# Kernel optimization log

Hardware: AMD Instinct MI355X
Metric: run time of the kernel (lower is better)

The kernel has to match this reference:

```python
import jax, jax.numpy as jnp
import numpy as np

N_HEAD = 16
N_KV_HEAD = 4
HEAD_DIM = 64
VE_CH = 12  # min(12, n_embd)


def apply_rotary_emb(x, cos, sin):
    d = x.shape[3] // 2
    x1, x2 = x[..., :d], x[..., d:]
    return jnp.concatenate([x1 * cos + x2 * sin, x1 * -sin + x2 * cos], axis=3)


def rms_norm(x):
    return x * jax.lax.rsqrt(jnp.mean(jnp.square(x), axis=-1, keepdims=True) + 1e-6)


def setup_inputs() -> dict:
    key = jax.random.key(0)
    ks = jax.random.split(key, 9)
    B, T, C = 2, 2048, 1024
    s = 0.02
    return {
        "x": jax.random.normal(ks[0], (B, T, C), jnp.float32),
        "ve": jax.random.normal(ks[1], (B, T, N_KV_HEAD * HEAD_DIM), jnp.float32),
        "cos": jax.random.normal(ks[2], (1, T, 1, HEAD_DIM // 2), jnp.float32),
        "sin": jax.random.normal(ks[3], (1, T, 1, HEAD_DIM // 2), jnp.float32),
        "Wq": jax.random.normal(ks[4], (C, C), jnp.float32) * s,
        "Wk": jax.random.normal(ks[5], (N_KV_HEAD * HEAD_DIM, C), jnp.float32) * s,
        "Wv": jax.random.normal(ks[6], (N_KV_HEAD * HEAD_DIM, C), jnp.float32) * s,
        "Wo": jax.random.normal(ks[7], (C, C), jnp.float32) * s,
        "Wg": jax.random.normal(ks[8], (N_KV_HEAD, VE_CH), jnp.float32) * s,
    }


def reference(x, ve, cos, sin, Wq, Wk, Wv, Wo, Wg):
    B, T, C = x.shape
    q = (x @ Wq.T).reshape(B, T, N_HEAD, HEAD_DIM)
    k = (x @ Wk.T).reshape(B, T, N_KV_HEAD, HEAD_DIM)
    v = (x @ Wv.T).reshape(B, T, N_KV_HEAD, HEAD_DIM)

    # value-embedding gate
    ve_r = ve.reshape(B, T, N_KV_HEAD, HEAD_DIM)
    gate = 3.0 * jax.nn.sigmoid(x[..., :VE_CH] @ Wg.T)  # [B,T,n_kv_head]
    v = v + gate[..., None] * ve_r

    q = apply_rotary_emb(q, cos, sin)
    k = apply_rotary_emb(k, cos, sin)
    q = rms_norm(q) * 1.2
    k = rms_norm(k) * 1.2

    # GQA: expand kv heads
    r = N_HEAD // N_KV_HEAD
    k = jnp.repeat(k, r, axis=2)
    v = jnp.repeat(v, r, axis=2)

    # [B,H,T,D]
    q = q.transpose(0, 2, 1, 3)
    k = k.transpose(0, 2, 1, 3)
    v = v.transpose(0, 2, 1, 3)

    scale = 1.0 / np.sqrt(HEAD_DIM).astype(np.float32)
    scores = jnp.einsum("bhqd,bhkd->bhqk", q, k) * scale
    causal = jnp.tril(jnp.ones((T, T), dtype=bool))
    scores = jnp.where(causal, scores, jnp.float32(-jnp.inf))
    att = jax.nn.softmax(scores, axis=-1)
    y = jnp.einsum("bhqk,bhkd->bhqd", att, v)
    y = y.transpose(0, 2, 1, 3).reshape(B, T, C)
    return y @ Wo.T
```

## Files before the change

kernel.cpp:

```cpp
#include <hip/hip_runtime.h>
#include <stdint.h>

#define B_SZ 2
#define T_SZ 2048
#define C_SZ 1024
#define NH   16
#define NKV  4
#define HD   64
#define KVD  256
#define QKV_N 1536

typedef __attribute__((ext_vector_type(8))) short bf16x8;
typedef __attribute__((ext_vector_type(4))) float f32x4;

#define GL(p) ((const __attribute__((address_space(1))) void*)(p))
#define LD(p) ((__attribute__((address_space(3))) void*)(p))

__device__ inline unsigned short f2bf(float f) {
  union { float f; unsigned u; } v; v.f = f;
  unsigned u = v.u;
  unsigned r = (u + 0x7fffu + ((u >> 16) & 1u)) >> 16;
  return (unsigned short)r;
}
__device__ inline unsigned short bftrunc(float f) {
  union { float f; unsigned u; } v; v.f = f;
  return (unsigned short)(v.u >> 16);
}

struct CvtArgs {
  const float *s0, *s1, *s2, *s3, *s4;
  unsigned short *d0, *d1, *d2, *d3, *d4;
  const float *x, *Wg;
  float *gate;
};
__global__ __launch_bounds__(256) void cvt_all(CvtArgs a) {
  int blk = blockIdx.x, tid = threadIdx.x;
  if (blk >= 6656) {
    int idx = (blk - 6656) * 256 + tid;
    int bt = idx >> 2, kh = idx & 3;
    float s = 0.f;
#pragma unroll
    for (int j = 0; j < 12; j++) s += a.x[(size_t)bt * C_SZ + j] * a.Wg[kh * 12 + j];
    a.gate[idx] = 3.f / (1.f + __expf(-s));
    return;
  }
  const float* s; unsigned short* d; int i;
  if      (blk < 4096) { s = a.s0; d = a.d0; i = blk * 256 + tid; }
  else if (blk < 5120) { s = a.s1; d = a.d1; i = (blk - 4096) * 256 + tid; }
  else if (blk < 5376) { s = a.s2; d = a.d2; i = (blk - 5120) * 256 + tid; }
  else if (blk < 5632) { s = a.s3; d = a.d3; i = (blk - 5376) * 256 + tid; }
  else                 { s = a.s4; d = a.d4; i = (blk - 5632) * 256 + tid; }
  float4 f = ((const float4*)s)[i];
  ushort4 o;
  o.x = f2bf(f.x); o.y = f2bf(f.y); o.z = f2bf(f.z); o.w = f2bf(f.w);
  ((ushort4*)d)[i] = o;
}

#define GEMM_PROLOG(A, Bm, K)                                                        \
  __shared__ unsigned short As[4][64 * 32];                                          \
  __shared__ unsigned short Bs[4][128 * 32];                                         \
  int tid  = threadIdx.x;                                                            \
  int lane = tid & 63;                                                               \
  int wave = tid >> 6;                                                               \
  int quad = lane >> 4;                                                              \
  int l16  = lane & 15;                                                              \
  int m0 = blockIdx.y * 64;                                                          \
  int n0 = blockIdx.x * 128;                                                         \
  int wm = (wave & 1) * 32;                                                          \
  int wn = (wave >> 1) * 64;                                                         \
  f32x4 acc[2][4];                                                                   \
  _Pragma("unroll") for (int i = 0; i < 2; i++)                                      \
    _Pragma("unroll") for (int j = 0; j < 4; j++)                                    \
      acc[i][j] = (f32x4){0.f, 0.f, 0.f, 0.f};                                       \
  int lrow = lane >> 2;                                                              \
  int lcol = (lane & 3) * 8;                                                         \
  int srowA = wave * 16;                                                             \
  int srowB = wave * 32;                                                             \
  const unsigned short* aP  = &A[(size_t)(m0 + srowA + lrow) * K + lcol];            \
  const unsigned short* b0P = &Bm[(size_t)(n0 + srowB + lrow) * K + lcol];           \
  const unsigned short* b1P = b0P + 16 * (size_t)K;                                  \
  for (int k0 = 0; k0 < K; k0 += 128) {                                              \
    __syncthreads();                                                                 \
    _Pragma("unroll") for (int p = 0; p < 4; p++) {                                  \
      __builtin_amdgcn_global_load_lds(GL(aP  + k0 + p * 32), LD(&As[p][srowA * 32]),        16, 0, 0); \
      __builtin_amdgcn_global_load_lds(GL(b0P + k0 + p * 32), LD(&Bs[p][srowB * 32]),        16, 0, 0); \
      __builtin_amdgcn_global_load_lds(GL(b1P + k0 + p * 32), LD(&Bs[p][(srowB + 16) * 32]), 16, 0, 0); \
    }                                                                                \
    __syncthreads();                                                                 \
    _Pragma("unroll") for (int p = 0; p < 4; p++) {                                  \
      bf16x8 af[2], bfr[4];                                                          \
      _Pragma("unroll") for (int i = 0; i < 2; i++)                                  \
        af[i] = *(const bf16x8*)&As[p][(wm + i * 16 + l16) * 32 + quad * 8];         \
      _Pragma("unroll") for (int j = 0; j < 4; j++)                                  \
        bfr[j] = *(const bf16x8*)&Bs[p][(wn + j * 16 + l16) * 32 + quad * 8];        \
      _Pragma("unroll") for (int i = 0; i < 2; i++)                                  \
        _Pragma("unroll") for (int j = 0; j < 4; j++)                                \
          acc[i][j] = __builtin_amdgcn_mfma_f32_16x16x32_bf16(af[i], bfr[j], acc[i][j], 0, 0, 0); \
    }                                                                                \
  }

__global__ __launch_bounds__(256) void gemm_bt(const unsigned short* __restrict__ A,
                                               const unsigned short* __restrict__ Bm,
                                               float* __restrict__ C,
                                               int N, int K) {
  GEMM_PROLOG(A, Bm, K)
#pragma unroll
  for (int i = 0; i < 2; i++) {
#pragma unroll
    for (int j = 0; j < 4; j++) {
      int col = n0 + wn + j * 16 + l16;
#pragma unroll
      for (int r = 0; r < 4; r++) {
        int row = m0 + wm + i * 16 + quad * 4 + r;
        C[(size_t)row * N + col] = acc[i][j][r];
      }
    }
  }
}

__global__ __launch_bounds__(256) void gemm_qkv(const unsigned short* __restrict__ A,
                                                const unsigned short* __restrict__ Bm,
                                                const float* __restrict__ ve,
                                                const float* __restrict__ cosb,
                                                const float* __restrict__ sinb,
                                                const float* __restrict__ gateArr,
                                                unsigned short* __restrict__ qa,
                                                unsigned short* __restrict__ ka,
                                                unsigned short* __restrict__ vtmp) {
  const int K = C_SZ;
  GEMM_PROLOG(A, Bm, K)

  int colbase = n0 + wn;
  if (colbase < 1280) {
    int isQ = colbase < 1024;
    int h   = isQ ? (colbase >> 6) : ((colbase - 1024) >> 6);
    float scale = isQ ? (0.15f * 1.44269504088896f) : 1.2f;
    unsigned short* dst = isQ ? qa : ka;
    int nheads = isQ ? NH : NKV;
#pragma unroll
    for (int i = 0; i < 2; i++) {
#pragma unroll
      for (int r = 0; r < 4; r++) {
        int row = m0 + wm + i * 16 + quad * 4 + r;
        int t = row & (T_SZ - 1), b = row >> 11;
        float a10 = acc[i][0][r], a11 = acc[i][1][r];
        float a20 = acc[i][2][r], a21 = acc[i][3][r];
        float cv0 = cosb[t * 32 + l16],      sv0 = sinb[t * 32 + l16];
        float cv1 = cosb[t * 32 + 16 + l16], sv1 = sinb[t * 32 + 16 + l16];
        float o10 =  a10 * cv0 + a20 * sv0;
        float o11 =  a11 * cv1 + a21 * sv1;
        float o20 = -a10 * sv0 + a20 * cv0;
        float o21 = -a11 * sv1 + a21 * cv1;
        float ssq = o10 * o10 + o11 * o11 + o20 * o20 + o21 * o21;
        ssq += __shfl_xor(ssq, 1);
        ssq += __shfl_xor(ssq, 2);
        ssq += __shfl_xor(ssq, 4);
        ssq += __shfl_xor(ssq, 8);
        float rn = rsqrtf(ssq * (1.f / 64.f) + 1e-6f) * scale;
        size_t base = ((size_t)(b * nheads + h) * T_SZ + t) * HD;
        dst[base + l16]      = f2bf(o10 * rn);
        dst[base + 16 + l16] = f2bf(o11 * rn);
        dst[base + 32 + l16] = f2bf(o20 * rn);
        dst[base + 48 + l16] = f2bf(o21 * rn);
      }
    }
  } else {
    int kh = (colbase - 1280) >> 6;
#pragma unroll
    for (int i = 0; i < 2; i++) {
#pragma unroll
      for (int r = 0; r < 4; r++) {
        int row = m0 + wm + i * 16 + quad * 4 + r;
        float g = gateArr[row * 4 + kh];
#pragma unroll
        for (int j = 0; j < 4; j++) {
          int d = j * 16 + l16;
          float val = acc[i][j][r] + g * ve[(size_t)row * KVD + kh * HD + d];
          vtmp[(size_t)row * KVD + kh * HD + d] = f2bf(val);
        }
      }
    }
  }
}

__global__ __launch_bounds__(256) void v_transpose(const unsigned short* __restrict__ vtmp,
                                                   unsigned short* __restrict__ vt) {
  __shared__ unsigned short tile[64 * 68];
  int blk = blockIdx.x;
  int tb = blk & 31, kh = (blk >> 5) & 3, b = blk >> 7;
  int tid = threadIdx.x;
  int r = tid >> 2, c = (tid & 3) * 16;
  const unsigned short* src = &vtmp[((size_t)(b * T_SZ + tb * 64 + r)) * KVD + kh * HD + c];
  uint4 x0 = *(const uint4*)(src);
  uint4 x1 = *(const uint4*)(src + 8);
  *(uint2*)&tile[r * 68 + c]      = *(uint2*)&x0;
  *(uint2*)&tile[r * 68 + c + 4]  = *((uint2*)&x0 + 1);
  *(uint2*)&tile[r * 68 + c + 8]  = *(uint2*)&x1;
  *(uint2*)&tile[r * 68 + c + 12] = *((uint2*)&x1 + 1);
  __syncthreads();
  int d = tid >> 2, tc = (tid & 3) * 16;
  ushort4 o0, o1, o2, o3;
  o0.x = tile[(tc + 0) * 68 + d];  o0.y = tile[(tc + 1) * 68 + d];
  o0.z = tile[(tc + 2) * 68 + d];  o0.w = tile[(tc + 3) * 68 + d];
  o1.x = tile[(tc + 4) * 68 + d];  o1.y = tile[(tc + 5) * 68 + d];
  o1.z = tile[(tc + 6) * 68 + d];  o1.w = tile[(tc + 7) * 68 + d];
  o2.x = tile[(tc + 8) * 68 + d];  o2.y = tile[(tc + 9) * 68 + d];
  o2.z = tile[(tc + 10) * 68 + d]; o2.w = tile[(tc + 11) * 68 + d];
  o3.x = tile[(tc + 12) * 68 + d]; o3.y = tile[(tc + 13) * 68 + d];
  o3.z = tile[(tc + 14) * 68 + d]; o3.w = tile[(tc + 15) * 68 + d];
  unsigned short* dst = &vt[((size_t)(b * NKV + kh) * HD + d) * T_SZ + tb * 64 + tc];
  *(ushort4*)(dst)      = o0;
  *(ushort4*)(dst + 4)  = o1;
  *(ushort4*)(dst + 8)  = o2;
  *(ushort4*)(dst + 12) = o3;
}

#define KST 72
#define PST 72
__global__ __launch_bounds__(256) void attn(const unsigned short* __restrict__ qa,
                                            const unsigned short* __restrict__ ka,
                                            const unsigned short* __restrict__ vt,
                                            unsigned short* __restrict__ y) {
  int bid = blockIdx.x;
  int half = bid >> 8, r = bid & 255;
  int qt = half ? (r & 15) : 15 - (r & 15);
  int bh = (half << 4) | (r >> 4);
  int b = bh >> 4, h = bh & 15;
  int kh = h >> 2;
  int tid = threadIdx.x;
  int wave = tid >> 6, lane = tid & 63;
  int quad = lane >> 4, l16 = lane & 15;

  __shared__ unsigned short Ks[2][64 * KST];
  __shared__ unsigned short Vs[2][64 * KST];
  __shared__ unsigned short Ps[128 * PST];
  unsigned short* Pw = &Ps[(wave * 32) * PST];

  bf16x8 bq[2][2];
#pragma unroll
  for (int qi = 0; qi < 2; qi++) {
    int tq = qt * 128 + wave * 32 + qi * 16 + l16;
    const unsigned short* qp = &qa[((size_t)(b * NH + h) * T_SZ + tq) * HD];
    bq[qi][0] = *(const bf16x8*)&qp[quad * 8];
    bq[qi][1] = *(const bf16x8*)&qp[32 + quad * 8];
  }

  const unsigned short one_bf = 0x3F80;
  bf16x8 vones = {(short)one_bf, (short)one_bf, (short)one_bf, (short)one_bf,
                  (short)one_bf, (short)one_bf, (short)one_bf, (short)one_bf};

  f32x4 oacc[2][4];
  f32x4 lacc[2];
#pragma unroll
  for (int qi = 0; qi < 2; qi++) {
    lacc[qi] = (f32x4){0.f, 0.f, 0.f, 0.f};
#pragma unroll
    for (int d = 0; d < 4; d++) oacc[qi][d] = (f32x4){0.f, 0.f, 0.f, 0.f};
  }

  int lr = tid >> 2;
  int lc = (tid & 3) * 16;

  const unsigned short* kbase = &ka[(size_t)(b * NKV + kh) * T_SZ * HD];
  const unsigned short* vbase = &vt[(size_t)(b * NKV + kh) * HD * T_SZ];

  int nj = 2 * qt + 2;

  {
    const unsigned short* kp = &kbase[(size_t)lr * HD + lc];
    const unsigned short* vp = &vbase[(size_t)lr * T_SZ + lc];
    uint4 k0 = *(const uint4*)(kp);
    uint4 k1 = *(const uint4*)(kp + 8);
    uint4 v0 = *(const uint4*)(vp);
    uint4 v1 = *(const uint4*)(vp + 8);
    *(uint4*)&Ks[0][lr * KST + lc]     = k0;
    *(uint4*)&Ks[0][lr * KST + lc + 8] = k1;
    *(uint4*)&Vs[0][lr * KST + lc]     = v0;
    *(uint4*)&Vs[0][lr * KST + lc + 8] = v1;
  }

  int qrow0 = qt * 128 + wave * 32;

  for (int j = 0; j < nj; j++) {
    int cur = j & 1, nxt = cur ^ 1;
    __syncthreads();

    uint4 k0, k1, v0, v1;
    bool pf = (j + 1 < nj);
    if (pf) {
      const unsigned short* kp = &kbase[(size_t)((j + 1) * 64 + lr) * HD + lc];
      const unsigned short* vp = &vbase[(size_t)lr * T_SZ + (j + 1) * 64 + lc];
      k0 = *(const uint4*)(kp);
      k1 = *(const uint4*)(kp + 8);
      v0 = *(const uint4*)(vp);
      v1 = *(const uint4*)(vp + 8);
    }

    f32x4 st[4][2];
#pragma unroll
    for (int tb = 0; tb < 4; tb++) {
      bf16x8 ak0 = *(const bf16x8*)&Ks[cur][(tb * 16 + l16) * KST + quad * 8];
      bf16x8 ak1 = *(const bf16x8*)&Ks[cur][(tb * 16 + l16) * KST + 32 + quad * 8];
#pragma unroll
      for (int qi = 0; qi < 2; qi++) {
        f32x4 s = (f32x4){0.f, 0.f, 0.f, 0.f};
        s = __builtin_amdgcn_mfma_f32_16x16x32_bf16(ak0, bq[qi][0], s, 0, 0, 0);
        s = __builtin_amdgcn_mfma_f32_16x16x32_bf16(ak1, bq[qi][1], s, 0, 0, 0);
        st[tb][qi] = s;
      }
    }

#pragma unroll
    for (int qi = 0; qi < 2; qi++) {
      int qlow = qrow0 + qi * 16;
      if (j * 64 + 63 > qlow) {
        int qg = qlow + l16;
#pragma unroll
        for (int tb = 0; tb < 4; tb++) {
          int tg = j * 64 + tb * 16 + quad * 4;
#pragma unroll
          for (int i = 0; i < 4; i++) {
            if (tg + i > qg) st[tb][qi][i] = -__builtin_inff();
          }
        }
      }
#pragma unroll
      for (int tb = 0; tb < 4; tb++) {
        ushort4 w;
        w.x = bftrunc(__builtin_amdgcn_exp2f(st[tb][qi][0]));
        w.y = bftrunc(__builtin_amdgcn_exp2f(st[tb][qi][1]));
        w.z = bftrunc(__builtin_amdgcn_exp2f(st[tb][qi][2]));
        w.w = bftrunc(__builtin_amdgcn_exp2f(st[tb][qi][3]));
        *(ushort4*)&Pw[(qi * 16 + l16) * PST + tb * 16 + quad * 4] = w;
      }
    }

    bf16x8 ap[2][2];
#pragma unroll
    for (int qi = 0; qi < 2; qi++) {
      ap[qi][0] = *(const bf16x8*)&Pw[(qi * 16 + l16) * PST + quad * 8];
      ap[qi][1] = *(const bf16x8*)&Pw[(qi * 16 + l16) * PST + 32 + quad * 8];
      lacc[qi] = __builtin_amdgcn_mfma_f32_16x16x32_bf16(ap[qi][0], vones, lacc[qi], 0, 0, 0);
      lacc[qi] = __builtin_amdgcn_mfma_f32_16x16x32_bf16(ap[qi][1], vones, lacc[qi], 0, 0, 0);
    }
#pragma unroll
    for (int d = 0; d < 4; d++) {
      bf16x8 bv0 = *(const bf16x8*)&Vs[cur][(d * 16 + l16) * KST + quad * 8];
      bf16x8 bv1 = *(const bf16x8*)&Vs[cur][(d * 16 + l16) * KST + 32 + quad * 8];
#pragma unroll
      for (int qi = 0; qi < 2; qi++) {
        oacc[qi][d] = __builtin_amdgcn_mfma_f32_16x16x32_bf16(ap[qi][0], bv0, oacc[qi][d], 0, 0, 0);
        oacc[qi][d] = __builtin_amdgcn_mfma_f32_16x16x32_bf16(ap[qi][1], bv1, oacc[qi][d], 0, 0, 0);
      }
    }

    if (pf) {
      *(uint4*)&Ks[nxt][lr * KST + lc]     = k0;
      *(uint4*)&Ks[nxt][lr * KST + lc + 8] = k1;
      *(uint4*)&Vs[nxt][lr * KST + lc]     = v0;
      *(uint4*)&Vs[nxt][lr * KST + lc + 8] = v1;
    }
  }

#pragma unroll
  for (int qi = 0; qi < 2; qi++) {
#pragma unroll
    for (int i = 0; i < 4; i++) {
      int tq = qrow0 + qi * 16 + quad * 4 + i;
      float inv = 1.f / lacc[qi][i];
#pragma unroll
      for (int d = 0; d < 4; d++) {
        y[((size_t)(b * T_SZ) + tq) * C_SZ + h * HD + d * 16 + l16] = f2bf(oacc[qi][d][i] * inv);
      }
    }
  }
}

extern "C" void kernel_launch(void* const* d_in, const int* in_sizes, int n_in,
                              void* d_out, int out_size, void* d_ws, size_t ws_size,
                              hipStream_t stream) {
  const float* x    = (const float*)d_in[0];
  const float* ve   = (const float*)d_in[1];
  const float* cosb = (const float*)d_in[2];
  const float* sinb = (const float*)d_in[3];
  const float* Wq   = (const float*)d_in[4];
  const float* Wk   = (const float*)d_in[5];
  const float* Wv   = (const float*)d_in[6];
  const float* Wo   = (const float*)d_in[7];
  const float* Wg   = (const float*)d_in[8];
  float* out = (float*)d_out;

  const size_t MB = 1024 * 1024;
  char* ws = (char*)d_ws;
  unsigned short* xb    = (unsigned short*)(ws);
  unsigned short* wqkvb = (unsigned short*)(ws + 8 * MB);
  unsigned short* wob   = (unsigned short*)(ws + 11 * MB);
  unsigned short* qab   = (unsigned short*)(ws + 13 * MB);
  unsigned short* kab   = (unsigned short*)(ws + 21 * MB);
  unsigned short* vtb   = (unsigned short*)(ws + 23 * MB);
  float*          gateA = (float*)(ws + 25 * MB);
  unsigned short* vtmp  = (unsigned short*)(ws + 26 * MB);
  unsigned short* yb    = xb;

  CvtArgs ca;
  ca.s0 = x;  ca.d0 = xb;
  ca.s1 = Wq; ca.d1 = wqkvb;
  ca.s2 = Wk; ca.d2 = wqkvb + 1024 * 1024;
  ca.s3 = Wv; ca.d3 = wqkvb + 1280 * 1024;
  ca.s4 = Wo; ca.d4 = wob;
  ca.x = x; ca.Wg = Wg; ca.gate = gateA;
  cvt_all<<<6720, 256, 0, stream>>>(ca);

  gemm_qkv<<<dim3(QKV_N / 128, (B_SZ * T_SZ) / 64), 256, 0, stream>>>(
      xb, wqkvb, ve, cosb, sinb, gateA, qab, kab, vtmp);

  v_transpose<<<256, 256, 0, stream>>>(vtmp, vtb);

  attn<<<512, 256, 0, stream>>>(qab, kab, vtb, yb);

  gemm_bt<<<dim3(C_SZ / 128, (B_SZ * T_SZ) / 64), 256, 0, stream>>>(
      yb, wob, out, C_SZ, C_SZ);
}
```

Baseline: 172.7 us.

## Double-buffer GEMM LDS tiles with XOR-swizzled layout and async prefetch

```diff
diff --git a/kernel.cpp b/kernel.cpp
--- a/kernel.cpp
+++ b/kernel.cpp
@@ -57,8 +57,8 @@
 }
 
 #define GEMM_PROLOG(A, Bm, K)                                                        \
-  __shared__ unsigned short As[4][64 * 32];                                          \
-  __shared__ unsigned short Bs[4][128 * 32];                                         \
+  __shared__ unsigned short As[2][64 * 64];                                          \
+  __shared__ unsigned short Bs[2][128 * 64];                                         \
   int tid  = threadIdx.x;                                                            \
   int lane = tid & 63;                                                               \
   int wave = tid >> 6;                                                               \
@@ -72,27 +72,42 @@
   _Pragma("unroll") for (int i = 0; i < 2; i++)                                      \
     _Pragma("unroll") for (int j = 0; j < 4; j++)                                    \
       acc[i][j] = (f32x4){0.f, 0.f, 0.f, 0.f};                                       \
-  int lrow = lane >> 2;                                                              \
-  int lcol = (lane & 3) * 8;                                                         \
-  int srowA = wave * 16;                                                             \
-  int srowB = wave * 32;                                                             \
-  const unsigned short* aP  = &A[(size_t)(m0 + srowA + lrow) * K + lcol];            \
-  const unsigned short* b0P = &Bm[(size_t)(n0 + srowB + lrow) * K + lcol];           \
-  const unsigned short* b1P = b0P + 16 * (size_t)K;                                  \
-  for (int k0 = 0; k0 < K; k0 += 128) {                                              \
+  int lrow = lane >> 3;                                 \
+  int lcol = ((lane & 7) ^ lrow) * 8;                 \
+  int sA = wave * 16;                                                                \
+  int sB = wave * 32;                                                                \
+  const unsigned short* aP0 = &A[(size_t)(m0 + sA + lrow) * K + lcol];               \
+  const unsigned short* aP1 = aP0 + 8 * (size_t)K;                                   \
+  const unsigned short* bP0 = &Bm[(size_t)(n0 + sB + lrow) * K + lcol];              \
+  const unsigned short* bP1 = bP0 + 8 * (size_t)K;                                   \
+  const unsigned short* bP2 = bP0 + 16 * (size_t)K;                                  \
+  const unsigned short* bP3 = bP0 + 24 * (size_t)K;                                  \
+  __builtin_amdgcn_global_load_lds(GL(aP0), LD(&As[0][(sA     ) * 64]), 16, 0, 0);   \
+  __builtin_amdgcn_global_load_lds(GL(aP1), LD(&As[0][(sA +  8) * 64]), 16, 0, 0);   \
+  __builtin_amdgcn_global_load_lds(GL(bP0), LD(&Bs[0][(sB     ) * 64]), 16, 0, 0);   \
+  __builtin_amdgcn_global_load_lds(GL(bP1), LD(&Bs[0][(sB +  8) * 64]), 16, 0, 0);   \
+  __builtin_amdgcn_global_load_lds(GL(bP2), LD(&Bs[0][(sB + 16) * 64]), 16, 0, 0);   \
+  __builtin_amdgcn_global_load_lds(GL(bP3), LD(&Bs[0][(sB + 24) * 64]), 16, 0, 0);   \
+  int swz = l16 & 7;                                                                 \
+  int nk = K >> 6;                                                                   \
+  for (int ki = 0; ki < nk; ki++) {                                                  \
+    int cur = ki & 1, nxt = cur ^ 1;                                                 \
     __syncthreads();                                                                 \
-    _Pragma("unroll") for (int p = 0; p < 4; p++) {                                  \
-      __builtin_amdgcn_global_load_lds(GL(aP  + k0 + p * 32), LD(&As[p][srowA * 32]),        16, 0, 0); \
-      __builtin_amdgcn_global_load_lds(GL(b0P + k0 + p * 32), LD(&Bs[p][srowB * 32]),        16, 0, 0); \
-      __builtin_amdgcn_global_load_lds(GL(b1P + k0 + p * 32), LD(&Bs[p][(srowB + 16) * 32]), 16, 0, 0); \
+    if (ki + 1 < nk) {                                                               \
+      int k0 = (ki + 1) << 6;                                                        \
+      __builtin_amdgcn_global_load_lds(GL(aP0 + k0), LD(&As[nxt][(sA     ) * 64]), 16, 0, 0); \
+      __builtin_amdgcn_global_load_lds(GL(aP1 + k0), LD(&As[nxt][(sA +  8) * 64]), 16, 0, 0); \
+      __builtin_amdgcn_global_load_lds(GL(bP0 + k0), LD(&Bs[nxt][(sB     ) * 64]), 16, 0, 0); \
+      __builtin_amdgcn_global_load_lds(GL(bP1 + k0), LD(&Bs[nxt][(sB +  8) * 64]), 16, 0, 0); \
+      __builtin_amdgcn_global_load_lds(GL(bP2 + k0), LD(&Bs[nxt][(sB + 16) * 64]), 16, 0, 0); \
+      __builtin_amdgcn_global_load_lds(GL(bP3 + k0), LD(&Bs[nxt][(sB + 24) * 64]), 16, 0, 0); \
     }                                                                                \
-    __syncthreads();                                                                 \
-    _Pragma("unroll") for (int p = 0; p < 4; p++) {                                  \
+    _Pragma("unroll") for (int p = 0; p < 2; p++) {                                  \
       bf16x8 af[2], bfr[4];                                                          \
       _Pragma("unroll") for (int i = 0; i < 2; i++)                                  \
-        af[i] = *(const bf16x8*)&As[p][(wm + i * 16 + l16) * 32 + quad * 8];         \
+        af[i] = *(const bf16x8*)&As[cur][(wm + i * 16 + l16) * 64 + (((p * 4 + quad) ^ swz) * 8)]; \
       _Pragma("unroll") for (int j = 0; j < 4; j++)                                  \
-        bfr[j] = *(const bf16x8*)&Bs[p][(wn + j * 16 + l16) * 32 + quad * 8];        \
+        bfr[j] = *(const bf16x8*)&Bs[cur][(wn + j * 16 + l16) * 64 + (((p * 4 + quad) ^ swz) * 8)]; \
       _Pragma("unroll") for (int i = 0; i < 2; i++)                                  \
         _Pragma("unroll") for (int j = 0; j < 4; j++)                                \
           acc[i][j] = __builtin_amdgcn_mfma_f32_16x16x32_bf16(af[i], bfr[j], acc[i][j], 0, 0, 0); \
```

Measured after the change: 170.1 us. About the same (-1.5%).
